# Kernel optimization log

Measured on AMD Instinct MI355X. Metric: run time of the kernel, lower is better.

## Reference

```python
import jax, jax.numpy as jnp
import numpy as np

T_STEPS, BATCH, DX, DH = 128, 128, 1024, 1024
N_GATES = 5


def setup_inputs() -> dict:
    key = jax.random.key(0)
    ks = jax.random.split(key, 4)
    scale_x = 1.0 / np.sqrt(DX)
    scale_h = 1.0 / np.sqrt(DH)
    inputs = jax.random.normal(ks[0], (T_STEPS, BATCH, DX), dtype=jnp.float32)
    memories = jax.random.normal(ks[1], (T_STEPS, BATCH, DH), dtype=jnp.float32)
    h0 = jnp.zeros((BATCH, DH), dtype=jnp.float32)
    c0 = jnp.zeros((BATCH, DH), dtype=jnp.float32)
    Wx = jax.random.normal(ks[2], (N_GATES * DH, DX), dtype=jnp.float32) * scale_x
    bx = jnp.zeros((N_GATES * DH,), dtype=jnp.float32)
    Wh = jax.random.normal(ks[3], (N_GATES * DH, DH), dtype=jnp.float32) * scale_h
    # forget-gate bias (second chunk) initialized to 1, as in reset_parameters_
    bh = jnp.zeros((N_GATES * DH,), dtype=jnp.float32).at[DH:2 * DH].set(1.0)
    return {"inputs": inputs, "memories": memories, "h0": h0, "c0": c0,
            "Wx": Wx, "bx": bx, "Wh": Wh, "bh": bh}


def reference(inputs, memories, h0, c0, Wx, bx, Wh, bh):
    # EpLSTMCell.loop: time-major scan of the custom gated cell.
    # Gate order: I, F, G, O, R (tied forget gate: it = 1 - ft).
    def step(carry, inp):
        h, c = carry
        xt, mt = inp
        gx = jnp.dot(xt, Wx.T) + bx      # [B, 5*Dh]
        gh = jnp.dot(h, Wh.T) + bh       # [B, 5*Dh]
        Xi, Xf, Xg, Xo, Xr = jnp.split(gx, N_GATES, axis=-1)
        Hi, Hf, Hg, Ho, Hr = jnp.split(gh, N_GATES, axis=-1)
        ft = jax.nn.sigmoid(Xf + Hf)
        ot = jax.nn.sigmoid(Xo + Ho)
        it = 1.0 - ft                    # tied forget gate
        gt = jnp.tanh(Xg + Hg)
        rt = jax.nn.sigmoid(Xr + Hr)     # episodic memory gate
        ct = ft * c + it * gt + rt * jnp.tanh(mt)
        ht = ot * jnp.tanh(ct)
        return (ht, ct), ht

    (_, _), outs = jax.lax.scan(step, (h0, c0), (inputs, memories))
    return outs  # [T, B, Dh]
```

## Files before the change

kernel.cpp:

```cpp
#include <hip/hip_runtime.h>

#define T_STEPS 128
#define BATCH   128
#define DX      1024
#define DH      1024
#define BDH     (BATCH * DH)
#define BDX     (BATCH * DX)
#define PLW     40

typedef __attribute__((ext_vector_type(8)))  short short8;
typedef __attribute__((ext_vector_type(16))) float f32x16;
typedef __attribute__((ext_vector_type(4)))  float f32x4v;
typedef __attribute__((ext_vector_type(2)))  float f32x2;
typedef __attribute__((ext_vector_type(4)))  unsigned u32x4;
typedef __attribute__((ext_vector_type(2)))  _Float16 f16x2;

static __device__ __forceinline__ unsigned short f2bf(float f) {
    union { float f; unsigned u; } v; v.f = f;
    unsigned r = v.u + 0x7fffu + ((v.u >> 16) & 1u);
    return (unsigned short)(r >> 16);
}
static __device__ __forceinline__ short8 pack_bf16x8(f32x4v lo, f32x4v hi) {
    union { unsigned short u[8]; short8 v; } pk;
    pk.u[0]=f2bf(lo[0]); pk.u[1]=f2bf(lo[1]); pk.u[2]=f2bf(lo[2]); pk.u[3]=f2bf(lo[3]);
    pk.u[4]=f2bf(hi[0]); pk.u[5]=f2bf(hi[1]); pk.u[6]=f2bf(hi[2]); pk.u[7]=f2bf(hi[3]);
    return pk.v;
}
static __device__ __forceinline__ float sigf(float x) {
    float u = __expf(-fabsf(x));
    float b = 1.0f / (1.0f + u);
    return x >= 0.0f ? b : 1.0f - b;
}
static __device__ __forceinline__ float tanhfast(float x) {
    float u = __expf(-2.0f * fabsf(x));
    float r = (1.0f - u) / (1.0f + u);
    return x >= 0.0f ? r : -r;
}


__global__ __launch_bounds__(256) void prep_x(const float* __restrict__ x,
                                              unsigned short* __restrict__ Xb) {
    const size_t i8 = ((size_t)blockIdx.x * 256 + threadIdx.x) * 8;
    f32x4v lo = __builtin_nontemporal_load((const f32x4v*)(x + i8));
    f32x4v hi = __builtin_nontemporal_load((const f32x4v*)(x + i8 + 4));
    short8 v = pack_bf16x8(lo, hi);
    __builtin_nontemporal_store(v, (short8*)(Xb + i8));
}

__global__ __launch_bounds__(256) void prep_tm(const float* __restrict__ mem,
                                               _Float16* __restrict__ TM) {
    const size_t i8 = ((size_t)blockIdx.x * 256 + threadIdx.x) * 8;
    f32x4v lo = __builtin_nontemporal_load((const f32x4v*)(mem + i8));
    f32x4v hi = __builtin_nontemporal_load((const f32x4v*)(mem + i8 + 4));
    union { _Float16 h[8]; u32x4 q; } V;
    #pragma unroll
    for (int j = 0; j < 4; ++j) V.h[j]     = (_Float16)tanhfast(lo[j]);
    #pragma unroll
    for (int j = 0; j < 4; ++j) V.h[4 + j] = (_Float16)tanhfast(hi[j]);
    __builtin_nontemporal_store(V.q, (u32x4*)(TM + i8));
}

__global__ __launch_bounds__(256) void init_seed(const float* __restrict__ h0,
                                                 unsigned short* __restrict__ hseq,
                                                 unsigned* __restrict__ gflag) {
    const int i = blockIdx.x * 256 + threadIdx.x;
    if (i < BDH) hseq[i] = f2bf(h0[i]);
    if (blockIdx.x < 2) gflag[blockIdx.x * 256 + threadIdx.x] = 0;
}

__global__ __launch_bounds__(256, 1) void eplstm_f(
    const unsigned short* __restrict__ Xb,
    const _Float16* __restrict__ TM,
    const float* __restrict__ Wx,
    const float* __restrict__ Wh,
    const float* __restrict__ bx,  const float* __restrict__ bh,
    const float* __restrict__ c0,
    unsigned short* __restrict__ hseq, float* __restrict__ out,
    unsigned* __restrict__ gflag)
{
    extern __shared__ char smem[];
    float* pl   = (float*)(smem + 65536);
    float* pl2a = (float*)(smem + 65536 + 20480);
    float* pl2b = (float*)(smem + 65536 + 40960);

    const int bid = blockIdx.x;
    const int js  = (bid >> 3) * 4 + (bid & 3);
    const int bhh = (bid >> 2) & 1;
    const int tid = threadIdx.x;

    const int wave = tid >> 6, lane = tid & 63;
    const int mh = wave >> 1, kh = wave & 1;
    const int arow = bhh * 64 + mh * 32 + (lane & 31);
    const int k8 = (lane >> 5) * 8;
    const int p = lane & 31;
    const int word = (p & 7) * 4 + (p >> 3);
    float* plw   = pl   + wave * 32 * PLW;
    float* pl2aw = pl2a + wave * 32 * PLW;
    float* pl2bw = pl2b + wave * 32 * PLW;
    unsigned long long* fb = (unsigned long long*)(gflag + bhh * 128);

    {
        const int row = tid >> 3;
        const int g = row >> 3, jj = row & 7;
        const int srow = (g + 1) * 1024 + js * 8 + jj;
        const int sw = (row & 7) << 4;
        const float* W = Wx + (size_t)srow * 1024;
        char* dst = smem + row * 2048;
        #pragma unroll
        for (int it = 0; it < 16; ++it) {
            const int k = (tid & 7) * 128 + it * 8;
            f32x4v lo = __builtin_nontemporal_load((const f32x4v*)(W + k));
            f32x4v hi = __builtin_nontemporal_load((const f32x4v*)(W + k + 4));
            short8 v = pack_bf16x8(lo, hi);
            *(short8*)(dst + ((k * 2) ^ sw)) = v;
        }
    }

    short8 breg[32];
    {
        const int r = lane & 31;
        const int g = r >> 3, jj = r & 7;
        const float* Wrow = Wh + (size_t)((g + 1) * 1024 + js * 8 + jj) * 1024
                          + kh * 512 + k8;
        #pragma unroll
        for (int ks = 0; ks < 32; ++ks) {
            f32x4v lo = *(const f32x4v*)(Wrow + ks * 16);
            f32x4v hi = *(const f32x4v*)(Wrow + ks * 16 + 4);
            breg[ks] = pack_bf16x8(lo, hi);
        }
    }

    const int e0 = tid * 2;
    const int row_e = e0 >> 3;
    const int jj0 = e0 & 7;
    const int brow = bhh * 64 + row_e;
    const size_t obase = (size_t)brow * DH + js * 8 + jj0;
    const int mh_e = row_e >> 5, r_e = row_e & 31;
    float biasv[2][4];
    #pragma unroll
    for (int e2 = 0; e2 < 2; ++e2)
        #pragma unroll
        for (int g = 0; g < 4; ++g) {
            const int srow = (g + 1) * 1024 + js * 8 + jj0 + e2;
            biasv[e2][g] = bx[srow] + bh[srow];
        }
    float2 creg = *(const float2*)(c0 + obase);

    const char* wrow = smem + (lane & 31) * 2048;
    const int sw2 = ((lane & 31) & 7) << 4;
    const int kbyte0 = (kh * 512 + k8) * 2;

    auto x_round = [&](int tt, float* slot) {
        const unsigned short* xp = Xb + (size_t)tt * BDX + (size_t)arow * DX
                                 + kh * 512 + k8;
        f32x16 xa0 = {}, xa1 = {};
        #pragma unroll 8
        for (int ks = 0; ks < 32; ++ks) {
            short8 a = *(const short8*)(xp + ks * 16);
            short8 b = *(const short8*)(wrow + ((kbyte0 + ks * 32) ^ sw2));
            if (ks & 1) xa1 = __builtin_amdgcn_mfma_f32_32x32x16_bf16(a, b, xa1, 0, 0, 0);
            else        xa0 = __builtin_amdgcn_mfma_f32_32x32x16_bf16(a, b, xa0, 0, 0, 0);
        }
        f32x16 xr = xa0 + xa1;
        #pragma unroll
        for (int ii = 0; ii < 16; ++ii) {
            const int rowc = (ii & 3) + 8 * (ii >> 2) + 4 * (lane >> 5);
            slot[rowc * PLW + word] = xr[ii];
        }
    };

    __syncthreads();

    x_round(0, pl2aw);
    x_round(1, pl2bw);

    for (int t = 0; t < T_STEPS; ++t) {
        f16x2 tm2 = __builtin_nontemporal_load(
            (const f16x2*)(TM + (size_t)t * BDH + obase));

        if (t > 0) {
            if (wave == 0) {
                for (;;) {
                    unsigned long long fv = __hip_atomic_load(
                        &fb[lane], __ATOMIC_RELAXED, __HIP_MEMORY_SCOPE_AGENT);
                    if (__all(((unsigned)fv >= (unsigned)t) &&
                              ((unsigned)(fv >> 32) >= (unsigned)t))) break;
                    __builtin_amdgcn_s_sleep(2);
                }
            }
            __syncthreads();
        }

        const unsigned short* hp = hseq + (size_t)t * BDH + (size_t)arow * DH + kh * 512 + k8;
        f32x16 a0 = {}, a1 = {};
        #pragma unroll
        for (int ks = 0; ks < 32; ++ks) {
            short8 a = *(const short8*)(hp + ks * 16);
            if (ks & 1) a1 = __builtin_amdgcn_mfma_f32_32x32x16_bf16(a, breg[ks], a1, 0, 0, 0);
            else        a0 = __builtin_amdgcn_mfma_f32_32x32x16_bf16(a, breg[ks], a0, 0, 0, 0);
        }
        f32x16 r = a0 + a1;
        #pragma unroll
        for (int ii = 0; ii < 16; ++ii) {
            const int rowc = (ii & 3) + 8 * (ii >> 2) + 4 * (lane >> 5);
            plw[rowc * PLW + word] = r[ii];
        }
        __syncthreads();

        const float* px = (t & 1) ? pl2b : pl2a;
        float4 h0A = *(const float4*)(pl + ((((mh_e << 1) | 0) * 32 + r_e) * PLW + (jj0 + 0) * 4));
        float4 h0B = *(const float4*)(pl + ((((mh_e << 1) | 1) * 32 + r_e) * PLW + (jj0 + 0) * 4));
        float4 h1A = *(const float4*)(pl + ((((mh_e << 1) | 0) * 32 + r_e) * PLW + (jj0 + 1) * 4));
        float4 h1B = *(const float4*)(pl + ((((mh_e << 1) | 1) * 32 + r_e) * PLW + (jj0 + 1) * 4));
        float4 x0A = *(const float4*)(px + ((((mh_e << 1) | 0) * 32 + r_e) * PLW + (jj0 + 0) * 4));
        float4 x0B = *(const float4*)(px + ((((mh_e << 1) | 1) * 32 + r_e) * PLW + (jj0 + 0) * 4));
        float4 x1A = *(const float4*)(px + ((((mh_e << 1) | 0) * 32 + r_e) * PLW + (jj0 + 1) * 4));
        float4 x1B = *(const float4*)(px + ((((mh_e << 1) | 1) * 32 + r_e) * PLW + (jj0 + 1) * 4));

        float hv[2];
        {
            const float gF = biasv[0][0] + h0A.x + h0B.x + x0A.x + x0B.x;
            const float gG = biasv[0][1] + h0A.y + h0B.y + x0A.y + x0B.y;
            const float gO = biasv[0][2] + h0A.z + h0B.z + x0A.z + x0B.z;
            const float gR = biasv[0][3] + h0A.w + h0B.w + x0A.w + x0B.w;
            const float ft = sigf(gF), ot = sigf(gO), rt = sigf(gR);
            const float gt = tanhfast(gG);
            const float cv = ft * creg.x + (1.f - ft) * gt + rt * (float)tm2[0];
            creg.x = cv;
            hv[0] = ot * tanhfast(cv);
        }
        {
            const float gF = biasv[1][0] + h1A.x + h1B.x + x1A.x + x1B.x;
            const float gG = biasv[1][1] + h1A.y + h1B.y + x1A.y + x1B.y;
            const float gO = biasv[1][2] + h1A.z + h1B.z + x1A.z + x1B.z;
            const float gR = biasv[1][3] + h1A.w + h1B.w + x1A.w + x1B.w;
            const float ft = sigf(gF), ot = sigf(gO), rt = sigf(gR);
            const float gt = tanhfast(gG);
            const float cv = ft * creg.y + (1.f - ft) * gt + rt * (float)tm2[1];
            creg.y = cv;
            hv[1] = ot * tanhfast(cv);
        }
        const unsigned hp2 = (unsigned)f2bf(hv[0]) | ((unsigned)f2bf(hv[1]) << 16);
        __hip_atomic_store((unsigned*)(hseq + (size_t)(t + 1) * BDH + obase), hp2,
                           __ATOMIC_RELAXED, __HIP_MEMORY_SCOPE_AGENT);
        asm volatile("s_waitcnt vmcnt(0)" ::: "memory");
        __syncthreads();
        if (tid == 0 && t < T_STEPS - 1) {
            __hip_atomic_store(&gflag[bhh * 128 + js], (unsigned)(t + 1),
                               __ATOMIC_RELAXED, __HIP_MEMORY_SCOPE_AGENT);
        }
        f32x2 hvv = { hv[0], hv[1] };
        __builtin_nontemporal_store(hvv, (f32x2*)(out + (size_t)t * BDH + obase));

        if (t + 2 < T_STEPS) x_round(t + 2, (t & 1) ? pl2bw : pl2aw);
    }
}

template<bool XBF16>
__global__ __launch_bounds__(256, 1) void eplstm_persistent(
    const void*  __restrict__ xsrc, const float* __restrict__ mem,
    const float* __restrict__ Wx,   const float* __restrict__ Wh,
    const float* __restrict__ bxp,  const float* __restrict__ bhp,
    const float* __restrict__ c0,
    unsigned short* __restrict__ hseq, float* __restrict__ out,
    unsigned* __restrict__ bar)
{
    extern __shared__ char smem[];
    float* pl = reinterpret_cast<float*>(smem + 131072);

    const int bid = blockIdx.x;
    const int js  = bid >> 1;
    const int bhh = bid & 1;
    const int tid = threadIdx.x;

    {
        const int prow = tid >> 3;
        const int g = prow >> 3, jj = prow & 7;
        const int srow = (g + 1) * 1024 + js * 8 + jj;
        const int kc = (tid & 7) * 256;
        const int sw = (prow & 7) << 4;
        for (int it = 0; it < 32; ++it) {
            const int k = kc + it * 8;
            const float* src = (k < DX) ? (Wx + (size_t)srow * DX + k)
                                        : (Wh + (size_t)srow * DH + (k - DX));
            f32x4v lo = *(const f32x4v*)(src);
            f32x4v hi = *(const f32x4v*)(src + 4);
            short8 v = pack_bf16x8(lo, hi);
            *reinterpret_cast<short8*>(smem + prow * 4096 + ((k * 2) ^ sw)) = v;
        }
    }

    const int e0   = tid * 2;
    const int bl   = e0 >> 3;
    const int jj0  = e0 & 7;
    const int brow_g = bhh * 64 + bl;
    const size_t oidx = (size_t)brow_g * DH + js * 8 + jj0;
    float biasv[2][4];
    #pragma unroll
    for (int e2 = 0; e2 < 2; ++e2)
        #pragma unroll
        for (int g = 0; g < 4; ++g) {
            const int srow = (g + 1) * 1024 + js * 8 + jj0 + e2;
            biasv[e2][g] = bxp[srow] + bhp[srow];
        }
    float2 creg = *reinterpret_cast<const float2*>(c0 + oidx);
    const int mh_e = bl >> 5, rr = bl & 31;

    const int wave = tid >> 6;
    const int lane = tid & 63;
    const int mh = wave >> 1, kh = wave & 1;
    const int arow   = bhh * 64 + mh * 32 + (lane & 31);
    const int k8     = (lane >> 5) * 8;
    const int brow   = lane & 31;
    const char* bbase = smem + brow * 4096;
    const int swz    = (brow & 7) << 4;
    const int kbyte0 = kh * 2048 + k8 * 2;

    __syncthreads();

    for (int t = 0; t < T_STEPS; ++t) {
        f32x16 ac0 = {}, ac1 = {}, ac2 = {}, ac3 = {};
        if (XBF16 || kh == 1) {
            const unsigned short* Ab = kh
                ? (hseq + (size_t)t * BDH + (size_t)arow * DH + k8)
                : ((const unsigned short*)xsrc + (size_t)t * BDX + (size_t)arow * DX + k8);
            #pragma unroll 8
            for (int ks = 0; ks < 64; ++ks) {
                short8 a = *reinterpret_cast<const short8*>(Ab + ks * 16);
                short8 b = *reinterpret_cast<const short8*>(bbase + ((kbyte0 + ks * 32) ^ swz));
                if      ((ks & 3) == 0) ac0 = __builtin_amdgcn_mfma_f32_32x32x16_bf16(a, b, ac0, 0, 0, 0);
                else if ((ks & 3) == 1) ac1 = __builtin_amdgcn_mfma_f32_32x32x16_bf16(a, b, ac1, 0, 0, 0);
                else if ((ks & 3) == 2) ac2 = __builtin_amdgcn_mfma_f32_32x32x16_bf16(a, b, ac2, 0, 0, 0);
                else                    ac3 = __builtin_amdgcn_mfma_f32_32x32x16_bf16(a, b, ac3, 0, 0, 0);
            }
        } else {
            const float* Af = (const float*)xsrc + (size_t)t * BDX + (size_t)arow * DX + k8;
            #pragma unroll 4
            for (int ks = 0; ks < 64; ++ks) {
                f32x4v lo = *(const f32x4v*)(Af + ks * 16);
                f32x4v hi = *(const f32x4v*)(Af + ks * 16 + 4);
                short8 a = pack_bf16x8(lo, hi);
                short8 b = *reinterpret_cast<const short8*>(bbase + ((kbyte0 + ks * 32) ^ swz));
                if      ((ks & 3) == 0) ac0 = __builtin_amdgcn_mfma_f32_32x32x16_bf16(a, b, ac0, 0, 0, 0);
                else if ((ks & 3) == 1) ac1 = __builtin_amdgcn_mfma_f32_32x32x16_bf16(a, b, ac1, 0, 0, 0);
                else if ((ks & 3) == 2) ac2 = __builtin_amdgcn_mfma_f32_32x32x16_bf16(a, b, ac2, 0, 0, 0);
                else                    ac3 = __builtin_amdgcn_mfma_f32_32x32x16_bf16(a, b, ac3, 0, 0, 0);
            }
        }
        f32x16 r = (ac0 + ac1) + (ac2 + ac3);

        #pragma unroll
        for (int i = 0; i < 16; ++i) {
            const int row = (i & 3) + 8 * (i >> 2) + 4 * (lane >> 5);
            pl[(wave * 32 + row) * 33 + brow] = r[i];
        }
        __syncthreads();

        const float2 mt2 = *reinterpret_cast<const float2*>(mem + (size_t)t * BDH + oidx);
        float hv[2];
        #pragma unroll
        for (int e2 = 0; e2 < 2; ++e2) {
            const int jj = jj0 + e2;
            float gs[4];
            #pragma unroll
            for (int g = 0; g < 4; ++g) {
                const int col = g * 8 + jj;
                gs[g] = pl[((mh_e * 2 + 0) * 32 + rr) * 33 + col]
                      + pl[((mh_e * 2 + 1) * 32 + rr) * 33 + col]
                      + biasv[e2][g];
            }
            const float ft = 1.f / (1.f + expf(-gs[0]));
            const float gt = tanhf(gs[1]);
            const float ot = 1.f / (1.f + expf(-gs[2]));
            const float rt = 1.f / (1.f + expf(-gs[3]));
            const float cin = e2 ? creg.y : creg.x;
            const float mvv = e2 ? mt2.y : mt2.x;
            const float cv = ft * cin + (1.f - ft) * gt + rt * tanhf(mvv);
            if (e2) creg.y = cv; else creg.x = cv;
            hv[e2] = ot * tanhf(cv);
        }
        *reinterpret_cast<float2*>(out + (size_t)t * BDH + oidx) = make_float2(hv[0], hv[1]);
        const unsigned hpk = (unsigned)f2bf(hv[0]) | ((unsigned)f2bf(hv[1]) << 16);
        __hip_atomic_store((unsigned*)(hseq + (size_t)(t + 1) * BDH + oidx), hpk,
                           __ATOMIC_RELAXED, __HIP_MEMORY_SCOPE_AGENT);

        __syncthreads();
        if (t < T_STEPS - 1) {
            if (tid == 0) {
                const unsigned want = (unsigned)(t + 1);
                const unsigned arrived = __hip_atomic_fetch_add(
                    &bar[bhh * 32], 1u, __ATOMIC_RELAXED, __HIP_MEMORY_SCOPE_AGENT);
                if (arrived == want * 128u - 1u) {
                    __hip_atomic_store(&bar[64 + bhh * 32], want,
                                       __ATOMIC_RELAXED, __HIP_MEMORY_SCOPE_AGENT);
                } else {
                    while (__hip_atomic_load(&bar[64 + bhh * 32],
                                             __ATOMIC_RELAXED, __HIP_MEMORY_SCOPE_AGENT) < want)
                        __builtin_amdgcn_s_sleep(2);
                }
            }
            __syncthreads();
        }
    }
}

extern "C" void kernel_launch(void* const* d_in, const int* in_sizes, int n_in,
                              void* d_out, int out_size, void* d_ws, size_t ws_size,
                              hipStream_t stream) {
    const float* inputs   = (const float*)d_in[0];
    const float* memories = (const float*)d_in[1];
    const float* h0       = (const float*)d_in[2];
    const float* c0       = (const float*)d_in[3];
    const float* Wx       = (const float*)d_in[4];
    const float* bx       = (const float*)d_in[5];
    const float* Wh       = (const float*)d_in[6];
    const float* bh_      = (const float*)d_in[7];
    float* outp = (float*)d_out;

    char* ws = (char*)d_ws;
    size_t off = 0;
    auto alloc = [&](size_t bytes) {
        char* p = ws + off;
        off = (off + bytes + 255) & ~(size_t)255;
        return p;
    };
    unsigned*       gflag = (unsigned*)alloc(512 * sizeof(unsigned));
    unsigned short* hseq  = (unsigned short*)alloc((size_t)(T_STEPS + 1) * BDH * 2);

    const size_t xb_b = (size_t)T_STEPS * BDX * 2;
    const size_t tm_b = (size_t)T_STEPS * BDH * 2;
    const size_t need_b = off + xb_b + 256 + tm_b + 256;

    if (ws_size >= need_b) {
        unsigned short* Xb = (unsigned short*)alloc(xb_b);
        _Float16*       TM = (_Float16*)alloc(tm_b);

        init_seed<<<512, 256, 0, stream>>>(h0, hseq, gflag);
        prep_x<<<8192, 256, 0, stream>>>(inputs, Xb);
        prep_tm<<<8192, 256, 0, stream>>>(memories, TM);

        const unsigned smem_bytes = 65536 + 3 * 4 * 32 * PLW * 4;
        (void)hipFuncSetAttribute((const void*)eplstm_f,
                                  hipFuncAttributeMaxDynamicSharedMemorySize, smem_bytes);
        void* kargs[] = { (void*)&Xb, (void*)&TM, (void*)&Wx, (void*)&Wh,
                          (void*)&bx, (void*)&bh_, (void*)&c0, (void*)&hseq,
                          (void*)&outp, (void*)&gflag };
        hipError_t err = hipLaunchCooperativeKernel((const void*)eplstm_f, dim3(256),
                                                    dim3(256), kargs, smem_bytes, stream);
        if (err != hipSuccess) {
            eplstm_f<<<256, 256, smem_bytes, stream>>>(Xb, TM, Wx, Wh, bx, bh_,
                                                       c0, hseq, outp, gflag);
        }
    } else {
        const bool use_xb = (ws_size >= off + xb_b + 256);
        unsigned short* Xb = use_xb ? (unsigned short*)alloc(xb_b) : nullptr;

        init_seed<<<512, 256, 0, stream>>>(h0, hseq, gflag);
        if (use_xb) prep_x<<<8192, 256, 0, stream>>>(inputs, Xb);

        const unsigned smem_bytes = 131072 + 9216 + 9216 + 64;
        const void* xsrc = use_xb ? (const void*)Xb : (const void*)inputs;
        if (use_xb) {
            (void)hipFuncSetAttribute((const void*)eplstm_persistent<true>,
                                      hipFuncAttributeMaxDynamicSharedMemorySize, smem_bytes);
            void* kargs[] = { (void*)&xsrc, (void*)&memories, (void*)&Wx, (void*)&Wh,
                              (void*)&bx, (void*)&bh_, (void*)&c0, (void*)&hseq,
                              (void*)&outp, (void*)&gflag };
            hipError_t err = hipLaunchCooperativeKernel(
                (const void*)eplstm_persistent<true>, dim3(256), dim3(256),
                kargs, smem_bytes, stream);
            if (err != hipSuccess) {
                eplstm_persistent<true><<<256, 256, smem_bytes, stream>>>(
                    xsrc, memories, Wx, Wh, bx, bh_, c0, hseq, outp, gflag);
            }
        } else {
            (void)hipFuncSetAttribute((const void*)eplstm_persistent<false>,
                                      hipFuncAttributeMaxDynamicSharedMemorySize, smem_bytes);
            void* kargs[] = { (void*)&xsrc, (void*)&memories, (void*)&Wx, (void*)&Wh,
                              (void*)&bx, (void*)&bh_, (void*)&c0, (void*)&hseq,
                              (void*)&outp, (void*)&gflag };
            hipError_t err = hipLaunchCooperativeKernel(
                (const void*)eplstm_persistent<false>, dim3(256), dim3(256),
                kargs, smem_bytes, stream);
            if (err != hipSuccess) {
                eplstm_persistent<false><<<256, 256, smem_bytes, stream>>>(
                    xsrc, memories, Wx, Wh, bx, bh_, c0, hseq, outp, gflag);
            }
        }
    }
}
```

Before: 1.641 ms.

## Hoist input projection into separate GEMM prepass and slim recurrent kernel

```diff
diff --git a/kernel.cpp b/kernel.cpp
--- a/kernel.cpp
+++ b/kernel.cpp
@@ -68,20 +68,114 @@
     if (blockIdx.x < 2) gflag[blockIdx.x * 256 + threadIdx.x] = 0;
 }
 
-__global__ __launch_bounds__(256, 1) void eplstm_f(
-    const unsigned short* __restrict__ Xb,
-    const _Float16* __restrict__ TM,
-    const float* __restrict__ Wx,
-    const float* __restrict__ Wh,
-    const float* __restrict__ bx,  const float* __restrict__ bh,
-    const float* __restrict__ c0,
+__global__ __launch_bounds__(256, 1) void gx_prepass4(
+    const unsigned short* __restrict__ Xb, const float* __restrict__ Wx,
+    const float* __restrict__ bx, const float* __restrict__ bh,
+    _Float16* __restrict__ Gx)
+{
+    extern __shared__ char sm[];
+    _Float16* pl16 = (_Float16*)(sm + 131072);
+
+    const int bid = blockIdx.x;
+    const int c  = bid & 7;
+    const int jp = bid >> 3;
+    const int tid = threadIdx.x;
+
+    {
+        const int row = tid >> 2;
+        const int chunk = tid & 3;
+        const int prow = jp * 64 + row;
+        const int srow = ((prow >> 3) & 3) * 1024 + 1024
+                       + (prow >> 5) * 8 + (prow & 7);
+        const int sw = (row & 7) << 4;
+        const float* W = Wx + (size_t)srow * DX + chunk * 256;
+        char* dst = sm + row * 2048;
+        #pragma unroll
+        for (int it = 0; it < 32; ++it) {
+            f32x4v lo = __builtin_nontemporal_load((const f32x4v*)(W + it * 8));
+            f32x4v hi = __builtin_nontemporal_load((const f32x4v*)(W + it * 8 + 4));
+            short8 v = pack_bf16x8(lo, hi);
+            *(short8*)(dst + (((chunk * 256 + it * 8) * 2) ^ sw)) = v;
+        }
+    }
+
+    const int rrow = tid >> 1;
+    const int jjb  = (tid & 1) * 4;
+    float bias_f[2][16];
+    #pragma unroll
+    for (int jsl = 0; jsl < 2; ++jsl)
+        #pragma unroll
+        for (int q = 0; q < 4; ++q)
+            #pragma unroll
+            for (int g = 0; g < 4; ++g) {
+                const int srow = (g + 1) * 1024 + (jp * 2 + jsl) * 8 + (jjb + q);
+                bias_f[jsl][q * 4 + g] = bx[srow] + bh[srow];
+            }
+
+    const int wave = tid >> 6, lane = tid & 63;
+    const int k8 = (lane >> 5) * 8;
+    const char* wrow0 = sm + (lane & 31) * 2048;
+    const char* wrow1 = wrow0 + 32 * 2048;
+    const int sw2 = ((lane & 31) & 7) << 4;
+    __syncthreads();
+
+    for (int i = 0; i < 16; ++i) {
+        const int mt = c * 16 + i;
+        const int arow = mt * 128 + wave * 32 + (lane & 31);
+        f32x16 a00 = {}, a01 = {}, a10 = {}, a11 = {};
+
+        const unsigned short* xp = Xb + (size_t)arow * 1024 + k8;
+        #pragma unroll 8
+        for (int ks = 0; ks < 64; ++ks) {
+            short8 a  = *(const short8*)(xp + ks * 16);
+            short8 b0 = *(const short8*)(wrow0 + ((ks * 32 + k8 * 2) ^ sw2));
+            short8 b1 = *(const short8*)(wrow1 + ((ks * 32 + k8 * 2) ^ sw2));
+            if (ks & 1) {
+                a01 = __builtin_amdgcn_mfma_f32_32x32x16_bf16(a, b0, a01, 0, 0, 0);
+                a11 = __builtin_amdgcn_mfma_f32_32x32x16_bf16(a, b1, a11, 0, 0, 0);
+            } else {
+                a00 = __builtin_amdgcn_mfma_f32_32x32x16_bf16(a, b0, a00, 0, 0, 0);
+                a10 = __builtin_amdgcn_mfma_f32_32x32x16_bf16(a, b1, a10, 0, 0, 0);
+            }
+        }
+        f32x16 r0 = a00 + a01;
+        f32x16 r1 = a10 + a11;
+
+        #pragma unroll
+        for (int ii = 0; ii < 16; ++ii) {
+            const int rowc = (ii & 3) + 8 * (ii >> 2) + 4 * (lane >> 5);
+            pl16[(wave * 32 + rowc) * 72 + (lane & 31)]      = (_Float16)r0[ii];
+            pl16[(wave * 32 + rowc) * 72 + 32 + (lane & 31)] = (_Float16)r1[ii];
+        }
+        __syncthreads();
+
+        #pragma unroll
+        for (int jsl = 0; jsl < 2; ++jsl) {
+            union { _Float16 h[16]; u32x4 q[2]; } V;
+            #pragma unroll
+            for (int q = 0; q < 4; ++q)
+                #pragma unroll
+                for (int g = 0; g < 4; ++g)
+                    V.h[q * 4 + g] = (_Float16)(
+                        (float)pl16[rrow * 72 + jsl * 32 + g * 8 + (jjb + q)]
+                        + bias_f[jsl][q * 4 + g]);
+            _Float16* dst = Gx + ((size_t)(mt * 128 + rrow) * 4096
+                                  + (jp * 2 + jsl) * 32 + jjb * 4);
+            __builtin_nontemporal_store(V.q[0], (u32x4*)dst);
+            __builtin_nontemporal_store(V.q[1], (u32x4*)(dst + 8));
+        }
+        __syncthreads();
+    }
+}
+
+__global__ __launch_bounds__(256, 1) void eplstm_h(
+    const _Float16* __restrict__ Gx,  const _Float16* __restrict__ TM,
+    const float* __restrict__ Wh,     const float* __restrict__ c0,
     unsigned short* __restrict__ hseq, float* __restrict__ out,
     unsigned* __restrict__ gflag)
 {
-    extern __shared__ char smem[];
-    float* pl   = (float*)(smem + 65536);
-    float* pl2a = (float*)(smem + 65536 + 20480);
-    float* pl2b = (float*)(smem + 65536 + 40960);
+    __shared__ float pl[2][4 * 32 * PLW];
+    __shared__ unsigned hdone;
 
     const int bid = blockIdx.x;
     const int js  = (bid >> 3) * 4 + (bid & 3);
@@ -94,27 +188,7 @@
     const int k8 = (lane >> 5) * 8;
     const int p = lane & 31;
     const int word = (p & 7) * 4 + (p >> 3);
-    float* plw   = pl   + wave * 32 * PLW;
-    float* pl2aw = pl2a + wave * 32 * PLW;
-    float* pl2bw = pl2b + wave * 32 * PLW;
-    unsigned long long* fb = (unsigned long long*)(gflag + bhh * 128);
-
-    {
-        const int row = tid >> 3;
-        const int g = row >> 3, jj = row & 7;
-        const int srow = (g + 1) * 1024 + js * 8 + jj;
-        const int sw = (row & 7) << 4;
-        const float* W = Wx + (size_t)srow * 1024;
-        char* dst = smem + row * 2048;
-        #pragma unroll
-        for (int it = 0; it < 16; ++it) {
-            const int k = (tid & 7) * 128 + it * 8;
-            f32x4v lo = __builtin_nontemporal_load((const f32x4v*)(W + k));
-            f32x4v hi = __builtin_nontemporal_load((const f32x4v*)(W + k + 4));
-            short8 v = pack_bf16x8(lo, hi);
-            *(short8*)(dst + ((k * 2) ^ sw)) = v;
-        }
-    }
+    const unsigned* fw = gflag + bhh * 128 + kh * 64;
 
     short8 breg[32];
     {
@@ -136,59 +210,24 @@
     const int brow = bhh * 64 + row_e;
     const size_t obase = (size_t)brow * DH + js * 8 + jj0;
     const int mh_e = row_e >> 5, r_e = row_e & 31;
-    float biasv[2][4];
-    #pragma unroll
-    for (int e2 = 0; e2 < 2; ++e2)
-        #pragma unroll
-        for (int g = 0; g < 4; ++g) {
-            const int srow = (g + 1) * 1024 + js * 8 + jj0 + e2;
-            biasv[e2][g] = bx[srow] + bh[srow];
-        }
     float2 creg = *(const float2*)(c0 + obase);
 
-    const char* wrow = smem + (lane & 31) * 2048;
-    const int sw2 = ((lane & 31) & 7) << 4;
-    const int kbyte0 = (kh * 512 + k8) * 2;
-
-    auto x_round = [&](int tt, float* slot) {
-        const unsigned short* xp = Xb + (size_t)tt * BDX + (size_t)arow * DX
-                                 + kh * 512 + k8;
-        f32x16 xa0 = {}, xa1 = {};
-        #pragma unroll 8
-        for (int ks = 0; ks < 32; ++ks) {
-            short8 a = *(const short8*)(xp + ks * 16);
-            short8 b = *(const short8*)(wrow + ((kbyte0 + ks * 32) ^ sw2));
-            if (ks & 1) xa1 = __builtin_amdgcn_mfma_f32_32x32x16_bf16(a, b, xa1, 0, 0, 0);
-            else        xa0 = __builtin_amdgcn_mfma_f32_32x32x16_bf16(a, b, xa0, 0, 0, 0);
-        }
-        f32x16 xr = xa0 + xa1;
-        #pragma unroll
-        for (int ii = 0; ii < 16; ++ii) {
-            const int rowc = (ii & 3) + 8 * (ii >> 2) + 4 * (lane >> 5);
-            slot[rowc * PLW + word] = xr[ii];
-        }
-    };
-
+    if (tid == 0) hdone = 0;
     __syncthreads();
 
-    x_round(0, pl2aw);
-    x_round(1, pl2bw);
-
     for (int t = 0; t < T_STEPS; ++t) {
+        u32x4 gxv = __builtin_nontemporal_load(
+            (const u32x4*)(Gx + ((size_t)(t * BATCH + brow) * 4096 + js * 32 + jj0 * 4)));
         f16x2 tm2 = __builtin_nontemporal_load(
             (const f16x2*)(TM + (size_t)t * BDH + obase));
 
         if (t > 0) {
-            if (wave == 0) {
-                for (;;) {
-                    unsigned long long fv = __hip_atomic_load(
-                        &fb[lane], __ATOMIC_RELAXED, __HIP_MEMORY_SCOPE_AGENT);
-                    if (__all(((unsigned)fv >= (unsigned)t) &&
-                              ((unsigned)(fv >> 32) >= (unsigned)t))) break;
-                    __builtin_amdgcn_s_sleep(2);
-                }
-            }
-            __syncthreads();
+            for (;;) {
+                unsigned f = __hip_atomic_load(&fw[lane], __ATOMIC_RELAXED,
+                                               __HIP_MEMORY_SCOPE_AGENT);
+                if (__all(f >= (unsigned)t)) break;
+                __builtin_amdgcn_s_sleep(1);
+            }
         }
 
         const unsigned short* hp = hseq + (size_t)t * BDH + (size_t)arow * DH + kh * 512 + k8;
@@ -200,6 +239,7 @@
             else        a0 = __builtin_amdgcn_mfma_f32_32x32x16_bf16(a, breg[ks], a0, 0, 0, 0);
         }
         f32x16 r = a0 + a1;
+        float* plw = &pl[t & 1][wave * 32 * PLW];
         #pragma unroll
         for (int ii = 0; ii < 16; ++ii) {
             const int rowc = (ii & 3) + 8 * (ii >> 2) + 4 * (lane >> 5);
@@ -207,22 +247,19 @@
         }
         __syncthreads();
 
-        const float* px = (t & 1) ? pl2b : pl2a;
-        float4 h0A = *(const float4*)(pl + ((((mh_e << 1) | 0) * 32 + r_e) * PLW + (jj0 + 0) * 4));
-        float4 h0B = *(const float4*)(pl + ((((mh_e << 1) | 1) * 32 + r_e) * PLW + (jj0 + 0) * 4));
-        float4 h1A = *(const float4*)(pl + ((((mh_e << 1) | 0) * 32 + r_e) * PLW + (jj0 + 1) * 4));
-        float4 h1B = *(const float4*)(pl + ((((mh_e << 1) | 1) * 32 + r_e) * PLW + (jj0 + 1) * 4));
-        float4 x0A = *(const float4*)(px + ((((mh_e << 1) | 0) * 32 + r_e) * PLW + (jj0 + 0) * 4));
-        float4 x0B = *(const float4*)(px + ((((mh_e << 1) | 1) * 32 + r_e) * PLW + (jj0 + 0) * 4));
-        float4 x1A = *(const float4*)(px + ((((mh_e << 1) | 0) * 32 + r_e) * PLW + (jj0 + 1) * 4));
-        float4 x1B = *(const float4*)(px + ((((mh_e << 1) | 1) * 32 + r_e) * PLW + (jj0 + 1) * 4));
+        const float* plr = pl[t & 1];
+        float4 h0A = *(const float4*)(plr + ((((mh_e << 1) | 0) * 32 + r_e) * PLW + (jj0 + 0) * 4));
+        float4 h0B = *(const float4*)(plr + ((((mh_e << 1) | 1) * 32 + r_e) * PLW + (jj0 + 0) * 4));
+        float4 h1A = *(const float4*)(plr + ((((mh_e << 1) | 0) * 32 + r_e) * PLW + (jj0 + 1) * 4));
+        float4 h1B = *(const float4*)(plr + ((((mh_e << 1) | 1) * 32 + r_e) * PLW + (jj0 + 1) * 4));
+        union { u32x4 u; _Float16 h[8]; } G; G.u = gxv;
 
         float hv[2];
         {
-            const float gF = biasv[0][0] + h0A.x + h0B.x + x0A.x + x0B.x;
-            const float gG = biasv[0][1] + h0A.y + h0B.y + x0A.y + x0B.y;
-            const float gO = biasv[0][2] + h0A.z + h0B.z + x0A.z + x0B.z;
-            const float gR = biasv[0][3] + h0A.w + h0B.w + x0A.w + x0B.w;
+            const float gF = (float)G.h[0] + h0A.x + h0B.x;
+            const float gG = (float)G.h[1] + h0A.y + h0B.y;
+            const float gO = (float)G.h[2] + h0A.z + h0B.z;
+            const float gR = (float)G.h[3] + h0A.w + h0B.w;
             const float ft = sigf(gF), ot = sigf(gO), rt = sigf(gR);
             const float gt = tanhfast(gG);
             const float cv = ft * creg.x + (1.f - ft) * gt + rt * (float)tm2[0];
@@ -230,10 +267,10 @@
             hv[0] = ot * tanhfast(cv);
         }
         {
-            const float gF = biasv[1][0] + h1A.x + h1B.x + x1A.x + x1B.x;
-            const float gG = biasv[1][1] + h1A.y + h1B.y + x1A.y + x1B.y;
-            const float gO = biasv[1][2] + h1A.z + h1B.z + x1A.z + x1B.z;
-            const float gR = biasv[1][3] + h1A.w + h1B.w + x1A.w + x1B.w;
+            const float gF = (float)G.h[4] + h1A.x + h1B.x;
+            const float gG = (float)G.h[5] + h1A.y + h1B.y;
+            const float gO = (float)G.h[6] + h1A.z + h1B.z;
+            const float gR = (float)G.h[7] + h1A.w + h1B.w;
             const float ft = sigf(gF), ot = sigf(gO), rt = sigf(gR);
             const float gt = tanhfast(gG);
             const float cv = ft * creg.y + (1.f - ft) * gt + rt * (float)tm2[1];
@@ -244,15 +281,14 @@
         __hip_atomic_store((unsigned*)(hseq + (size_t)(t + 1) * BDH + obase), hp2,
                            __ATOMIC_RELAXED, __HIP_MEMORY_SCOPE_AGENT);
         asm volatile("s_waitcnt vmcnt(0)" ::: "memory");
-        __syncthreads();
-        if (tid == 0 && t < T_STEPS - 1) {
+        const unsigned old = __hip_atomic_fetch_add(&hdone, 1u, __ATOMIC_RELAXED,
+                                                    __HIP_MEMORY_SCOPE_WORKGROUP);
+        if ((old & 3u) == 3u && t < T_STEPS - 1) {
             __hip_atomic_store(&gflag[bhh * 128 + js], (unsigned)(t + 1),
                                __ATOMIC_RELAXED, __HIP_MEMORY_SCOPE_AGENT);
         }
         f32x2 hvv = { hv[0], hv[1] };
         __builtin_nontemporal_store(hvv, (f32x2*)(out + (size_t)t * BDH + obase));
-
-        if (t + 2 < T_STEPS) x_round(t + 2, (t & 1) ? pl2bw : pl2aw);
     }
 }
 
@@ -429,27 +465,29 @@
 
     const size_t xb_b = (size_t)T_STEPS * BDX * 2;
     const size_t tm_b = (size_t)T_STEPS * BDH * 2;
-    const size_t need_b = off + xb_b + 256 + tm_b + 256;
+    const size_t gx_b = (size_t)16384 * 4096 * 2;
+    const size_t need_b = off + xb_b + 256 + tm_b + 256 + gx_b + 256;
 
     if (ws_size >= need_b) {
         unsigned short* Xb = (unsigned short*)alloc(xb_b);
         _Float16*       TM = (_Float16*)alloc(tm_b);
+        _Float16*       Gx = (_Float16*)alloc(gx_b);
 
         init_seed<<<512, 256, 0, stream>>>(h0, hseq, gflag);
         prep_x<<<8192, 256, 0, stream>>>(inputs, Xb);
         prep_tm<<<8192, 256, 0, stream>>>(memories, TM);
 
-        const unsigned smem_bytes = 65536 + 3 * 4 * 32 * PLW * 4;
-        (void)hipFuncSetAttribute((const void*)eplstm_f,
-                                  hipFuncAttributeMaxDynamicSharedMemorySize, smem_bytes);
-        void* kargs[] = { (void*)&Xb, (void*)&TM, (void*)&Wx, (void*)&Wh,
-                          (void*)&bx, (void*)&bh_, (void*)&c0, (void*)&hseq,
-                          (void*)&outp, (void*)&gflag };
-        hipError_t err = hipLaunchCooperativeKernel((const void*)eplstm_f, dim3(256),
-                                                    dim3(256), kargs, smem_bytes, stream);
+        const unsigned pre_smem = 131072 + 128 * 72 * 2;
+        (void)hipFuncSetAttribute((const void*)gx_prepass4,
+                                  hipFuncAttributeMaxDynamicSharedMemorySize, pre_smem);
+        gx_prepass4<<<512, 256, pre_smem, stream>>>(Xb, Wx, bx, bh_, Gx);
+
+        void* kargs[] = { (void*)&Gx, (void*)&TM, (void*)&Wh, (void*)&c0,
+                          (void*)&hseq, (void*)&outp, (void*)&gflag };
+        hipError_t err = hipLaunchCooperativeKernel((const void*)eplstm_h, dim3(256),
+                                                    dim3(256), kargs, 0, stream);
         if (err != hipSuccess) {
-            eplstm_f<<<256, 256, smem_bytes, stream>>>(Xb, TM, Wx, Wh, bx, bh_,
-                                                       c0, hseq, outp, gflag);
+            eplstm_h<<<256, 256, 0, stream>>>(Gx, TM, Wh, c0, hseq, outp, gflag);
         }
     } else {
         const bool use_xb = (ws_size >= off + xb_b + 256);
```

After: 2.384 ms. 1.45x slower.
